# Performance work log

Measured on AMD Instinct MI355X. Metric: run time of the kernel, lower is better.

## Reference

```python
import jax, jax.numpy as jnp
import numpy as np
import math

B, S, D = 4096, 16, 256
HS, HT, O = 512, 512, 1


def setup_inputs() -> dict:
    key = jax.random.key(0)
    ks = jax.random.split(key, 20)
    stdv_s = 1.0 / math.sqrt(HS)
    stdv_t = 1.0 / math.sqrt(HT)
    u = lambda k, shape, s: jax.random.uniform(k, shape, jnp.float32, -s, s)
    return {
        "X": jax.random.normal(ks[0], (B, S, D), jnp.float32),
        # SpatialLSTM params (init uniform(-1/sqrt(H), 1/sqrt(H)) as in torch)
        "sa_W": u(ks[1], (D, 4 * HS), stdv_s),
        "sa_U": u(ks[2], (HS, 4 * HS), stdv_s),
        "sa_b": u(ks[3], (4 * HS,), stdv_s),
        "sa_Wa": u(ks[4], (D, D), stdv_s),
        "sa_Ua": u(ks[5], (2 * HS, D), stdv_s),
        "sa_ba": u(ks[6], (D,), stdv_s),
        "sa_Va": u(ks[7], (D, D), stdv_s),
        # TemporalLSTM params
        "ta_Wa": u(ks[8], (HS, S), stdv_t),
        "ta_Ua": u(ks[9], (HT, S), stdv_t),
        "ta_ba": u(ks[10], (S,), stdv_t),
        "ta_Va": u(ks[11], (S, S), stdv_t),
        "ta_W": u(ks[12], (HS, 4 * HT), stdv_t),
        "ta_U": u(ks[13], (HT, 4 * HT), stdv_t),
        "ta_b": u(ks[14], (4 * HT,), stdv_t),
        "ta_Wy": u(ks[15], (O, 4 * HT), stdv_t),
        "fc_W": u(ks[16], (O, HT), stdv_t),
        "fc_b": u(ks[17], (O,), stdv_t),
    }


def _lstm_update(gates, c, H):
    i = jax.nn.sigmoid(gates[:, :H])
    f = jax.nn.sigmoid(gates[:, H:2 * H])
    g = jnp.tanh(gates[:, 2 * H:3 * H])
    o = jax.nn.sigmoid(gates[:, 3 * H:])
    c_new = f * c + i * g
    h_new = o * jnp.tanh(c_new)
    return h_new, c_new


def _forward(X, sa_W, sa_U, sa_b, sa_Wa, sa_Ua, sa_ba, sa_Va,
             ta_Wa, ta_Ua, ta_ba, ta_Va, ta_W, ta_U, ta_b, ta_Wy, fc_W, fc_b):
    batch = X.shape[0]
    x = X  # x = X[:, :, 0:input_dim] == full X
    y0 = X[:, 0, D - 1:D]  # y = X[:, :, input_dim-1:], take t=0 -> [B, 1]

    # ---- Spatial attention LSTM over time ----
    def sa_step(carry, x_t):
        h, c = carry
        hc = jnp.concatenate([h, c], axis=1)  # [B, 2*HS]
        a_t = jnp.tanh(x_t @ sa_Wa + hc @ sa_Ua + sa_ba) @ sa_Va  # [B, D]
        alpha_t = jax.nn.softmax(a_t, axis=1)
        xt = alpha_t * x_t
        gates = xt @ sa_W + h @ sa_U + sa_b  # [B, 4*HS]
        h, c = _lstm_update(gates, c, HS)
        return (h, c), h

    h0 = jnp.zeros((batch, HS), X.dtype)
    c0 = jnp.zeros((batch, HS), X.dtype)
    _, hseq = jax.lax.scan(sa_step, (h0, c0), jnp.swapaxes(x, 0, 1))  # [S, B, HS]
    H3 = jnp.swapaxes(hseq, 0, 1)  # [B, S, HS]

    # ---- Temporal attention LSTM ----
    s0 = jnp.zeros((batch, HT), X.dtype)  # s_t is never updated in the original code

    def ta_step(carry, h_t):
        lh, lc, y_prev = carry
        beta = jnp.tanh(h_t @ ta_Wa + s0 @ ta_Ua + ta_ba) @ ta_Va  # [B, S]
        beta = jax.nn.softmax(beta, axis=1)
        h_ctx = jnp.einsum('bs,bsh->bh', beta, H3)  # [B, HS]
        gates = h_ctx @ ta_W + lh @ ta_U + y_prev @ ta_Wy + ta_b  # [B, 4*HT]
        lh, lc = _lstm_update(gates, lc, HT)
        y = lh @ fc_W.T + fc_b  # [B, O]
        return (lh, lc, y), None

    (_, _, y_pred), _ = jax.lax.scan(ta_step, (h0[:, :HT] * 0.0, c0[:, :HT] * 0.0, y0), hseq)
    return y_pred  # [B, O]


def reference(X, sa_W, sa_U, sa_b, sa_Wa, sa_Ua, sa_ba, sa_Va,
              ta_Wa, ta_Ua, ta_ba, ta_Va, ta_W, ta_U, ta_b, ta_Wy, fc_W, fc_b):
    return _forward(X, sa_W, sa_U, sa_b, sa_Wa, sa_Ua, sa_ba, sa_Va,
                    ta_Wa, ta_Ua, ta_ba, ta_Va, ta_W, ta_U, ta_b, ta_Wy, fc_W, fc_b)
```

## Files before the change

kernel.cpp:

```cpp
#include <hip/hip_runtime.h>


constexpr int Bb = 4096;
constexpr int Ss = 16;
constexpr int Dd = 256;
constexpr int Hh = 512;

typedef __attribute__((ext_vector_type(8))) short short8;
typedef __attribute__((ext_vector_type(4))) float f32x4;

__device__ __forceinline__ float sigm(float x) { return 1.0f / (1.0f + expf(-x)); }

__device__ __forceinline__ unsigned short f2bf(float x) {
    unsigned int u = __float_as_uint(x);
    u = (u + 0x7fffu + ((u >> 16) & 1u)) >> 16;
    return (unsigned short)u;
}
__device__ __forceinline__ float bf2f(unsigned short h) {
    return __uint_as_float(((unsigned int)h) << 16);
}
__device__ __forceinline__ void async16(const void* g, void* l) {
    __builtin_amdgcn_global_load_lds(
        (const __attribute__((address_space(1))) void*)g,
        (__attribute__((address_space(3))) void*)l, 16, 0, 0);
}

struct SegB { const unsigned short* Ah; const unsigned short* Al;
              const unsigned short* Bh; const unsigned short* Bl;
              int lda; int ldb; int K; };

template<int BM, int BN, int NSEG, int EPI>
__global__ __launch_bounds__(256) void gemm_mfma_k(
    SegB s0, SegB s1, SegB s2,
    const float* __restrict__ bias,
    float* __restrict__ C,
    unsigned short* __restrict__ Th, unsigned short* __restrict__ Tl,
    int ldc)
{
    constexpr int WM = BM / 2, WN = BN / 2;
    constexpr int FI = WM / 16, FJ = WN / 16;
    __shared__ __align__(16) unsigned short sA[2][BM * 32];
    __shared__ __align__(16) unsigned short sB[2][BN * 32];
    const int tid  = threadIdx.x;
    const int lane = tid & 63;
    const int wv   = tid >> 6;
    const int wm   = wv & 1, wn = wv >> 1;
    const int row0 = blockIdx.x * BM;
    const int col0 = blockIdx.y * BN;

    f32x4 acc[FI][FJ];
#pragma unroll
    for (int i = 0; i < FI; i++)
#pragma unroll
        for (int j = 0; j < FJ; j++) acc[i][j] = (f32x4){0.f, 0.f, 0.f, 0.f};

    const int lrow = lane >> 2;
    const int lcol = (lane & 3) * 8;
    const int q8   = (lane >> 4) * 8;
    const int l15  = lane & 15;

#pragma unroll
    for (int sgi = 0; sgi < NSEG; ++sgi) {
        const SegB sg = (sgi == 0) ? s0 : ((sgi == 1) ? s1 : s2);
        const int K = sg.K;
        for (int k0 = 0; k0 < K; k0 += 32) {
#pragma unroll
            for (int c = wv; c < BM / 16; c += 4) {
                const int r = c * 16 + lrow;
                const size_t gA = (size_t)(row0 + r) * sg.lda + k0 + lcol;
                const int lo = c * 512 + lane * 8;
                async16(sg.Ah + gA, &sA[0][lo]);
                async16(sg.Al + gA, &sA[1][lo]);
            }
#pragma unroll
            for (int c = wv; c < BN / 16; c += 4) {
                const int r = c * 16 + lrow;
                const size_t gB = (size_t)(col0 + r) * sg.ldb + k0 + lcol;
                const int lo = c * 512 + lane * 8;
                async16(sg.Bh + gB, &sB[0][lo]);
                async16(sg.Bl + gB, &sB[1][lo]);
            }
            __syncthreads();
            short8 ah[FI], al[FI], bh[FJ], bl[FJ];
#pragma unroll
            for (int i = 0; i < FI; i++) {
                const int m = wm * WM + i * 16 + l15;
                ah[i] = *reinterpret_cast<const short8*>(&sA[0][m * 32 + q8]);
                al[i] = *reinterpret_cast<const short8*>(&sA[1][m * 32 + q8]);
            }
#pragma unroll
            for (int j = 0; j < FJ; j++) {
                const int n = wn * WN + j * 16 + l15;
                bh[j] = *reinterpret_cast<const short8*>(&sB[0][n * 32 + q8]);
                bl[j] = *reinterpret_cast<const short8*>(&sB[1][n * 32 + q8]);
            }
#pragma unroll
            for (int i = 0; i < FI; i++)
#pragma unroll
                for (int j = 0; j < FJ; j++) {
                    acc[i][j] = __builtin_amdgcn_mfma_f32_16x16x32_bf16(ah[i], bh[j], acc[i][j], 0, 0, 0);
                    acc[i][j] = __builtin_amdgcn_mfma_f32_16x16x32_bf16(ah[i], bl[j], acc[i][j], 0, 0, 0);
                    acc[i][j] = __builtin_amdgcn_mfma_f32_16x16x32_bf16(al[i], bh[j], acc[i][j], 0, 0, 0);
                }
            __syncthreads();
        }
    }
#pragma unroll
    for (int i = 0; i < FI; i++) {
#pragma unroll
        for (int j = 0; j < FJ; j++) {
            const int col = col0 + wn * WN + j * 16 + l15;
#pragma unroll
            for (int r = 0; r < 4; r++) {
                const int row = row0 + wm * WM + i * 16 + (lane >> 4) * 4 + r;
                float v = acc[i][j][r];
                if (EPI == 1) {
                    v = tanhf(v + bias[col]);
                    unsigned short hb = f2bf(v);
                    Th[(size_t)row * ldc + col] = hb;
                    Tl[(size_t)row * ldc + col] = f2bf(v - bf2f(hb));
                } else {
                    C[(size_t)row * ldc + col] = v;
                }
            }
        }
    }
}

__global__ __launch_bounds__(256) void splitT_k(const float* __restrict__ W,
                                                unsigned short* __restrict__ Th,
                                                unsigned short* __restrict__ Tl,
                                                int Kd, int Nd)
{
    __shared__ float tile[32][33];
    const int bk = blockIdx.x * 32, bn = blockIdx.y * 32;
    const int tid = threadIdx.x;
    const int r = tid >> 3, c4 = (tid & 7) * 4;
    const float4 v = *reinterpret_cast<const float4*>(&W[(size_t)(bk + r) * Nd + bn + c4]);
    tile[r][c4 + 0] = v.x; tile[r][c4 + 1] = v.y;
    tile[r][c4 + 2] = v.z; tile[r][c4 + 3] = v.w;
    __syncthreads();
    const int n = r, k4 = c4;
    ushort4 hq, lq;
    unsigned short* hp = (unsigned short*)&hq;
    unsigned short* lp = (unsigned short*)&lq;
#pragma unroll
    for (int q = 0; q < 4; q++) {
        float x = tile[k4 + q][n];
        unsigned short h = f2bf(x);
        hp[q] = h;
        lp[q] = f2bf(x - bf2f(h));
    }
    *reinterpret_cast<ushort4*>(&Th[(size_t)(bn + n) * Kd + bk + k4]) = hq;
    *reinterpret_cast<ushort4*>(&Tl[(size_t)(bn + n) * Kd + bk + k4]) = lq;
}

__global__ __launch_bounds__(256) void init_k(const float* __restrict__ X,
                                              unsigned short* __restrict__ xsh,
                                              unsigned short* __restrict__ xsl,
                                              float* __restrict__ yv)
{
    int idx = blockIdx.x * 256 + threadIdx.x;
    int b = idx >> 8, d = idx & 255;
    float xv = X[(size_t)b * (Ss * Dd) + d];
    unsigned short hb = f2bf(xv);
    xsh[idx] = hb;
    xsl[idx] = f2bf(xv - bf2f(hb));
    if (d == Dd - 1) yv[b] = xv;
}

__global__ __launch_bounds__(256) void softmax_xt_k(const float* __restrict__ a,
                                                    const float* __restrict__ X,
                                                    unsigned short* __restrict__ xh,
                                                    unsigned short* __restrict__ xl,
                                                    int t)
{
    int b = blockIdx.x, tid = threadIdx.x;
    __shared__ float red[256];
    float v = a[(size_t)b * Dd + tid];
    red[tid] = v; __syncthreads();
    for (int s = 128; s > 0; s >>= 1) {
        if (tid < s) red[tid] = fmaxf(red[tid], red[tid + s]);
        __syncthreads();
    }
    float mx = red[0]; __syncthreads();
    float e = expf(v - mx);
    red[tid] = e; __syncthreads();
    for (int s = 128; s > 0; s >>= 1) {
        if (tid < s) red[tid] += red[tid + s];
        __syncthreads();
    }
    float inv = 1.0f / red[0];
    float xv = e * inv * X[(size_t)b * Ss * Dd + (size_t)t * Dd + tid];
    unsigned short h = f2bf(xv);
    xh[(size_t)b * Dd + tid] = h;
    xl[(size_t)b * Dd + tid] = f2bf(xv - bf2f(h));
}

template<int ZC, int SPLITX>
__global__ __launch_bounds__(256) void lstm_sa_k(
    const float* __restrict__ gates, const float* __restrict__ bias,
    float* __restrict__ c_io,
    unsigned short* __restrict__ h3h, unsigned short* __restrict__ h3l,
    unsigned short* __restrict__ ch, unsigned short* __restrict__ cl,
    const float* __restrict__ X,
    unsigned short* __restrict__ xsh, unsigned short* __restrict__ xsl,
    int tnext)
{
    int idx = blockIdx.x * 256 + threadIdx.x;
    int b = idx >> 9, j = idx & 511;
    const float* g = gates + (size_t)b * 4 * Hh;
    float gi = g[j]          + bias[j];
    float gf = g[Hh + j]     + bias[Hh + j];
    float gg = g[2 * Hh + j] + bias[2 * Hh + j];
    float go = g[3 * Hh + j] + bias[3 * Hh + j];
    float i_ = sigm(gi), f_ = sigm(gf), gv = tanhf(gg), o_ = sigm(go);
    float cp = ZC ? 0.0f : c_io[idx];
    float c = f_ * cp + i_ * gv;
    c_io[idx] = c;
    unsigned short cb = f2bf(c);
    ch[idx] = cb;
    cl[idx] = f2bf(c - bf2f(cb));
    float h = o_ * tanhf(c);
    unsigned short hb = f2bf(h);
    h3h[idx] = hb;
    h3l[idx] = f2bf(h - bf2f(hb));
    if (SPLITX && j < Dd) {
        float xv = X[(size_t)b * (Ss * Dd) + (size_t)tnext * Dd + j];
        unsigned short xb = f2bf(xv);
        xsh[(size_t)b * Dd + j] = xb;
        xsl[(size_t)b * Dd + j] = f2bf(xv - bf2f(xb));
    }
}

template<int ZC>
__global__ __launch_bounds__(512) void lstm_ta_k(const float* __restrict__ gates,
                                                 const float* __restrict__ bias,
                                                 const float* __restrict__ wy,
                                                 const float* __restrict__ fcW,
                                                 const float* __restrict__ fcb,
                                                 float* __restrict__ yv,
                                                 float* __restrict__ c_io,
                                                 unsigned short* __restrict__ hh,
                                                 unsigned short* __restrict__ hl,
                                                 float* __restrict__ outp)
{
    int b = blockIdx.x, j = threadIdx.x;
    size_t idx = (size_t)b * Hh + j;
    const float* g = gates + (size_t)b * 4 * Hh;
    float yb = yv[b];
    float gi = g[j]          + bias[j]          + yb * wy[j];
    float gf = g[Hh + j]     + bias[Hh + j]     + yb * wy[Hh + j];
    float gg = g[2 * Hh + j] + bias[2 * Hh + j] + yb * wy[2 * Hh + j];
    float go = g[3 * Hh + j] + bias[3 * Hh + j] + yb * wy[3 * Hh + j];
    float i_ = sigm(gi), f_ = sigm(gf), gv = tanhf(gg), o_ = sigm(go);
    float cp = ZC ? 0.0f : c_io[idx];
    float c = f_ * cp + i_ * gv;
    c_io[idx] = c;
    float h = o_ * tanhf(c);
    unsigned short hb = f2bf(h);
    hh[idx] = hb;
    hl[idx] = f2bf(h - bf2f(hb));
    float p = h * fcW[j];
#pragma unroll
    for (int off = 32; off > 0; off >>= 1) p += __shfl_down(p, off, 64);
    __shared__ float wred[8];
    if ((j & 63) == 0) wred[j >> 6] = p;
    __syncthreads();
    if (j == 0) {
        float y = fcb[0];
#pragma unroll
        for (int w = 0; w < 8; w++) y += wred[w];
        yv[b] = y;
        if (outp) outp[b] = y;
    }
}

__global__ __launch_bounds__(256) void beta_k(const unsigned short* __restrict__ H3h,
                                              const unsigned short* __restrict__ H3l,
                                              const float* __restrict__ taWa,
                                              const float* __restrict__ taba,
                                              const float* __restrict__ taVa,
                                              float* __restrict__ beta)
{
    int bx = blockIdx.x, t = blockIdx.y, tid = threadIdx.x;
    __shared__ float Was[512 * 16];
    __shared__ float red[16 * 16 * 16];
    __shared__ float Vas[256];
    __shared__ float tt[16][17];
    __shared__ float lt[16][17];
    for (int i = tid; i < 512 * 16; i += 256) Was[i] = taWa[i];
    Vas[tid] = taVa[tid];
    __syncthreads();
    const int r = tid >> 4, c = tid & 15;
    const int b = bx * 16 + r;
    const unsigned short* hrh = H3h + ((size_t)t * Bb + b) * Hh + c * 32;
    const unsigned short* hrl = H3l + ((size_t)t * Bb + b) * Hh + c * 32;
    float acc[16];
#pragma unroll
    for (int n = 0; n < 16; n++) acc[n] = 0.0f;
    for (int k = 0; k < 32; k++) {
        float hk = bf2f(hrh[k]) + bf2f(hrl[k]);
        const float* w = &Was[(c * 32 + k) * 16];
#pragma unroll
        for (int n = 0; n < 16; n++) acc[n] = fmaf(hk, w[n], acc[n]);
    }
#pragma unroll
    for (int n = 0; n < 16; n++) red[(r * 16 + n) * 16 + c] = acc[n];
    __syncthreads();
    float s = 0.0f;
#pragma unroll
    for (int cc = 0; cc < 16; cc++) s += red[(r * 16 + c) * 16 + cc];
    tt[r][c] = tanhf(s + taba[c]);
    __syncthreads();
    float l = 0.0f;
#pragma unroll
    for (int m = 0; m < 16; m++) l = fmaf(tt[r][m], Vas[m * 16 + c], l);
    lt[r][c] = l;
    __syncthreads();
    float mx = -1e30f;
#pragma unroll
    for (int m = 0; m < 16; m++) mx = fmaxf(mx, lt[r][m]);
    float sum = 0.0f;
#pragma unroll
    for (int m = 0; m < 16; m++) sum += expf(lt[r][m] - mx);
    beta[((size_t)t * Bb + b) * 16 + c] = expf(l - mx) / sum;
}

__global__ __launch_bounds__(256) void hctx_all_k(unsigned short* __restrict__ H3h,
                                                  unsigned short* __restrict__ H3l,
                                                  const float* __restrict__ beta)
{
    int b = blockIdx.x, tid = threadIdx.x;
    __shared__ float Hs[16][516];
    __shared__ float bs[16][16];
    for (int i = tid; i < 16 * 512; i += 256) {
        int s = i >> 9, h = i & 511;
        size_t o = ((size_t)s * Bb + b) * Hh + h;
        Hs[s][h] = bf2f(H3h[o]) + bf2f(H3l[o]);
    }
    {
        int t = tid >> 4, s = tid & 15;
        bs[t][s] = beta[((size_t)t * Bb + b) * 16 + s];
    }
    __syncthreads();
#pragma unroll
    for (int t = 0; t < 16; t++) {
        for (int h = tid; h < Hh; h += 256) {
            float a = 0.0f;
#pragma unroll
            for (int s = 0; s < 16; s++) a = fmaf(bs[t][s], Hs[s][h], a);
            unsigned short hb = f2bf(a);
            size_t o = ((size_t)t * Bb + b) * Hh + h;
            H3h[o] = hb;
            H3l[o] = f2bf(a - bf2f(hb));
        }
    }
}

extern "C" void kernel_launch(void* const* d_in, const int* in_sizes, int n_in,
                              void* d_out, int out_size, void* d_ws, size_t ws_size,
                              hipStream_t stream)
{
    (void)in_sizes; (void)n_in; (void)out_size; (void)ws_size;
    const float* X     = (const float*)d_in[0];
    const float* sa_W  = (const float*)d_in[1];
    const float* sa_U  = (const float*)d_in[2];
    const float* sa_b  = (const float*)d_in[3];
    const float* sa_Wa = (const float*)d_in[4];
    const float* sa_Ua = (const float*)d_in[5];
    const float* sa_ba = (const float*)d_in[6];
    const float* sa_Va = (const float*)d_in[7];
    const float* ta_Wa = (const float*)d_in[8];
    const float* ta_ba = (const float*)d_in[10];
    const float* ta_Va = (const float*)d_in[11];
    const float* ta_W  = (const float*)d_in[12];
    const float* ta_U  = (const float*)d_in[13];
    const float* ta_b  = (const float*)d_in[14];
    const float* ta_Wy = (const float*)d_in[15];
    const float* fc_W  = (const float*)d_in[16];
    const float* fc_b  = (const float*)d_in[17];

    char* base = (char*)d_ws;
    size_t off = 0;
    auto alloc = [&](size_t bytes) {
        void* p = base + off; off += (bytes + 255) & ~(size_t)255; return p;
    };
    const size_t BH = (size_t)Bb * Hh;
    float* gates = (float*)alloc(BH * 4 * 4);
    float* avxt  = gates;
    unsigned short* H3h = (unsigned short*)alloc((size_t)Ss * BH * 2);
    unsigned short* H3l = (unsigned short*)alloc((size_t)Ss * BH * 2);
    float* cbuf = (float*)alloc(BH * 4);
    float* lc   = (float*)alloc(BH * 4);
    unsigned short* xth = (unsigned short*)alloc((size_t)Bb * Dd * 2);
    unsigned short* xtl = (unsigned short*)alloc((size_t)Bb * Dd * 2);
    unsigned short* xsh = (unsigned short*)alloc((size_t)Bb * Dd * 2);
    unsigned short* xsl = (unsigned short*)alloc((size_t)Bb * Dd * 2);
    unsigned short* ch  = (unsigned short*)alloc(BH * 2);
    unsigned short* cl  = (unsigned short*)alloc(BH * 2);
    unsigned short* tmph = (unsigned short*)alloc((size_t)Bb * Dd * 2);
    unsigned short* tmpl = (unsigned short*)alloc((size_t)Bb * Dd * 2);
    unsigned short* saWth = (unsigned short*)alloc((size_t)Dd * 4 * Hh * 2);
    unsigned short* saWtl = (unsigned short*)alloc((size_t)Dd * 4 * Hh * 2);
    unsigned short* saUth = (unsigned short*)alloc((size_t)Hh * 4 * Hh * 2);
    unsigned short* saUtl = (unsigned short*)alloc((size_t)Hh * 4 * Hh * 2);
    unsigned short* taWth = (unsigned short*)alloc((size_t)Hh * 4 * Hh * 2);
    unsigned short* taWtl = (unsigned short*)alloc((size_t)Hh * 4 * Hh * 2);
    unsigned short* taUth = (unsigned short*)alloc((size_t)Hh * 4 * Hh * 2);
    unsigned short* taUtl = (unsigned short*)alloc((size_t)Hh * 4 * Hh * 2);
    unsigned short* WaTh = (unsigned short*)alloc((size_t)Dd * Dd * 2);
    unsigned short* WaTl = (unsigned short*)alloc((size_t)Dd * Dd * 2);
    unsigned short* UaTh = (unsigned short*)alloc((size_t)2 * Hh * Dd * 2);
    unsigned short* UaTl = (unsigned short*)alloc((size_t)2 * Hh * Dd * 2);
    unsigned short* VaTh = (unsigned short*)alloc((size_t)Dd * Dd * 2);
    unsigned short* VaTl = (unsigned short*)alloc((size_t)Dd * Dd * 2);
    float* yv = (float*)alloc((size_t)Bb * 4);
    float* beta = (float*)xth;
    unsigned short* lhh = (unsigned short*)cbuf;
    unsigned short* lhl = (unsigned short*)cbuf + BH;

    splitT_k<<<dim3(Dd / 32, (4 * Hh) / 32), 256, 0, stream>>>(sa_W, saWth, saWtl, Dd, 4 * Hh);
    splitT_k<<<dim3(Hh / 32, (4 * Hh) / 32), 256, 0, stream>>>(sa_U, saUth, saUtl, Hh, 4 * Hh);
    splitT_k<<<dim3(Hh / 32, (4 * Hh) / 32), 256, 0, stream>>>(ta_W, taWth, taWtl, Hh, 4 * Hh);
    splitT_k<<<dim3(Hh / 32, (4 * Hh) / 32), 256, 0, stream>>>(ta_U, taUth, taUtl, Hh, 4 * Hh);
    splitT_k<<<dim3(Dd / 32, Dd / 32), 256, 0, stream>>>(sa_Wa, WaTh, WaTl, Dd, Dd);
    splitT_k<<<dim3((2 * Hh) / 32, Dd / 32), 256, 0, stream>>>(sa_Ua, UaTh, UaTl, 2 * Hh, Dd);
    splitT_k<<<dim3(Dd / 32, Dd / 32), 256, 0, stream>>>(sa_Va, VaTh, VaTl, Dd, Dd);
    init_k<<<dim3((Bb * Dd) / 256), 256, 0, stream>>>(X, xsh, xsl, yv);

    const dim3 agrid(Bb / 64, Dd / 64);
    const dim3 ggrid(Bb / 128, (4 * Hh) / 128);

    for (int t = 0; t < Ss; ++t) {
        SegB a0{ xsh, xsl, WaTh, WaTl, Dd, Dd, Dd };
        if (t == 0) {
            gemm_mfma_k<64, 64, 1, 1><<<agrid, 256, 0, stream>>>(
                a0, a0, a0, sa_ba, nullptr, tmph, tmpl, Dd);
        } else {
            SegB a1{ H3h + (size_t)(t - 1) * BH, H3l + (size_t)(t - 1) * BH,
                     UaTh, UaTl, Hh, 2 * Hh, Hh };
            SegB a2{ ch, cl, UaTh + Hh, UaTl + Hh, Hh, 2 * Hh, Hh };
            gemm_mfma_k<64, 64, 3, 1><<<agrid, 256, 0, stream>>>(
                a0, a1, a2, sa_ba, nullptr, tmph, tmpl, Dd);
        }

        SegB v0{ tmph, tmpl, VaTh, VaTl, Dd, Dd, Dd };
        gemm_mfma_k<64, 64, 1, 0><<<agrid, 256, 0, stream>>>(
            v0, v0, v0, nullptr, avxt, nullptr, nullptr, Dd);

        softmax_xt_k<<<Bb, 256, 0, stream>>>(avxt, X, xth, xtl, t);

        SegB g0{ xth, xtl, saWth, saWtl, Dd, Dd, Dd };
        if (t == 0) {
            gemm_mfma_k<128, 128, 1, 0><<<ggrid, 256, 0, stream>>>(
                g0, g0, g0, nullptr, gates, nullptr, nullptr, 4 * Hh);
            lstm_sa_k<1, 1><<<(int)(BH / 256), 256, 0, stream>>>(
                gates, sa_b, cbuf, H3h + (size_t)t * BH, H3l + (size_t)t * BH,
                ch, cl, X, xsh, xsl, t + 1);
        } else {
            SegB g1{ H3h + (size_t)(t - 1) * BH, H3l + (size_t)(t - 1) * BH,
                     saUth, saUtl, Hh, Hh, Hh };
            gemm_mfma_k<128, 128, 2, 0><<<ggrid, 256, 0, stream>>>(
                g0, g1, g1, nullptr, gates, nullptr, nullptr, 4 * Hh);
            if (t < Ss - 1)
                lstm_sa_k<0, 1><<<(int)(BH / 256), 256, 0, stream>>>(
                    gates, sa_b, cbuf, H3h + (size_t)t * BH, H3l + (size_t)t * BH,
                    ch, cl, X, xsh, xsl, t + 1);
            else
                lstm_sa_k<0, 0><<<(int)(BH / 256), 256, 0, stream>>>(
                    gates, sa_b, cbuf, H3h + (size_t)t * BH, H3l + (size_t)t * BH,
                    ch, cl, X, xsh, xsl, 0);
        }
    }

    beta_k<<<dim3(Bb / 16, Ss), 256, 0, stream>>>(H3h, H3l, ta_Wa, ta_ba, ta_Va, beta);
    hctx_all_k<<<Bb, 256, 0, stream>>>(H3h, H3l, beta);

    for (int t = 0; t < Ss; ++t) {
        SegB g0{ H3h + (size_t)t * BH, H3l + (size_t)t * BH,
                 taWth, taWtl, Hh, Hh, Hh };
        if (t == 0) {
            gemm_mfma_k<128, 128, 1, 0><<<ggrid, 256, 0, stream>>>(
                g0, g0, g0, nullptr, gates, nullptr, nullptr, 4 * Hh);
            lstm_ta_k<1><<<Bb, 512, 0, stream>>>(
                gates, ta_b, ta_Wy, fc_W, fc_b, yv, lc, lhh, lhl,
                (t == Ss - 1) ? (float*)d_out : nullptr);
        } else {
            SegB g1{ lhh, lhl, taUth, taUtl, Hh, Hh, Hh };
            gemm_mfma_k<128, 128, 2, 0><<<ggrid, 256, 0, stream>>>(
                g0, g1, g1, nullptr, gates, nullptr, nullptr, 4 * Hh);
            lstm_ta_k<0><<<Bb, 512, 0, stream>>>(
                gates, ta_b, ta_Wy, fc_W, fc_b, yv, lc, lhh, lhl,
                (t == Ss - 1) ? (float*)d_out : nullptr);
        }
    }
}
```

Baseline: 2.916 ms.

## Fuse LSTM gate GEMMs with cell update epilogue and MFMA-ize temporal attention

Adds a gate GEMM kernel whose tile interleaves the four gate columns for each hidden unit, so the LSTM cell update runs in the epilogue. This removes the fp32 gates buffer round trip and the separate lstm kernels for both recurrences. The temporal attention beta computation now uses split-bf16 MFMA over 128-row tiles with a pre-transposed Wa, and the x split-copy moves into the softmax kernel. The temporal hidden state is double-buffered because the fused kernel reads the previous h while writing the new one, and a small y_k kernel computes the fc output. The cost is a larger per-thread epilogue and a narrow 32-column tile.

```diff
diff --git a/kernel.cpp b/kernel.cpp
--- a/kernel.cpp
+++ b/kernel.cpp
@@ -122,6 +122,121 @@
                 } else {
                     C[(size_t)row * ldc + col] = v;
                 }
+            }
+        }
+    }
+}
+
+template<int NSEG, int ZC, int TA>
+__global__ __launch_bounds__(256) void gemm_gates_k(
+    SegB s0, SegB s1,
+    const float* __restrict__ bias,
+    const float* __restrict__ wy,
+    const float* __restrict__ yv,
+    float* __restrict__ c_io,
+    unsigned short* __restrict__ hh, unsigned short* __restrict__ hl,
+    unsigned short* __restrict__ ch, unsigned short* __restrict__ cl)
+{
+    __shared__ __align__(16) unsigned short sA[2][128 * 32];
+    __shared__ __align__(16) unsigned short sB[2][128 * 32];
+    const int tid  = threadIdx.x;
+    const int lane = tid & 63;
+    const int wv   = tid >> 6;
+    const int wm   = wv & 1, wn = wv >> 1;
+    const int row0 = blockIdx.x * 128;
+    const int by32 = blockIdx.y * 32;
+
+    f32x4 acc[4][4];
+#pragma unroll
+    for (int i = 0; i < 4; i++)
+#pragma unroll
+        for (int g = 0; g < 4; g++) acc[i][g] = (f32x4){0.f, 0.f, 0.f, 0.f};
+
+    const int lrow = lane >> 2;
+    const int lcol = (lane & 3) * 8;
+    const int q8   = (lane >> 4) * 8;
+    const int l15  = lane & 15;
+
+#pragma unroll
+    for (int sgi = 0; sgi < NSEG; ++sgi) {
+        const SegB sg = (sgi == 0) ? s0 : s1;
+        const int K = sg.K;
+        for (int k0 = 0; k0 < K; k0 += 32) {
+#pragma unroll
+            for (int c = wv; c < 8; c += 4) {
+                const int r = c * 16 + lrow;
+                const size_t gA = (size_t)(row0 + r) * sg.lda + k0 + lcol;
+                const int lo = c * 512 + lane * 8;
+                async16(sg.Ah + gA, &sA[0][lo]);
+                async16(sg.Al + gA, &sA[1][lo]);
+            }
+#pragma unroll
+            for (int cc = wv; cc < 8; cc += 4) {
+                const int g  = cc >> 1;
+                const int jj = (cc & 1) * 16 + lrow;
+                const int rowg = g * 512 + by32 + jj;
+                const size_t gB = (size_t)rowg * sg.ldb + k0 + lcol;
+                const int lo = cc * 512 + lane * 8;
+                async16(sg.Bh + gB, &sB[0][lo]);
+                async16(sg.Bl + gB, &sB[1][lo]);
+            }
+            __syncthreads();
+            short8 ah[4], al[4], bh[4], bl[4];
+#pragma unroll
+            for (int i = 0; i < 4; i++) {
+                const int m = wm * 64 + i * 16 + l15;
+                ah[i] = *reinterpret_cast<const short8*>(&sA[0][m * 32 + q8]);
+                al[i] = *reinterpret_cast<const short8*>(&sA[1][m * 32 + q8]);
+            }
+#pragma unroll
+            for (int g = 0; g < 4; g++) {
+                const int n = g * 32 + wn * 16 + l15;
+                bh[g] = *reinterpret_cast<const short8*>(&sB[0][n * 32 + q8]);
+                bl[g] = *reinterpret_cast<const short8*>(&sB[1][n * 32 + q8]);
+            }
+#pragma unroll
+            for (int i = 0; i < 4; i++)
+#pragma unroll
+                for (int g = 0; g < 4; g++) {
+                    acc[i][g] = __builtin_amdgcn_mfma_f32_16x16x32_bf16(ah[i], bh[g], acc[i][g], 0, 0, 0);
+                    acc[i][g] = __builtin_amdgcn_mfma_f32_16x16x32_bf16(ah[i], bl[g], acc[i][g], 0, 0, 0);
+                    acc[i][g] = __builtin_amdgcn_mfma_f32_16x16x32_bf16(al[i], bh[g], acc[i][g], 0, 0, 0);
+                }
+            __syncthreads();
+        }
+    }
+    const int j = by32 + wn * 16 + l15;
+    const float b0 = bias[j],            b1 = bias[Hh + j];
+    const float b2 = bias[2 * Hh + j],   b3 = bias[3 * Hh + j];
+    float w0 = 0.f, w1 = 0.f, w2 = 0.f, w3 = 0.f;
+    if (TA) { w0 = wy[j]; w1 = wy[Hh + j]; w2 = wy[2 * Hh + j]; w3 = wy[3 * Hh + j]; }
+#pragma unroll
+    for (int i = 0; i < 4; i++) {
+        const int rbase = row0 + wm * 64 + i * 16 + (lane >> 4) * 4;
+#pragma unroll
+        for (int r = 0; r < 4; r++) {
+            const int row = rbase + r;
+            float gi = acc[i][0][r] + b0;
+            float gf = acc[i][1][r] + b1;
+            float gg = acc[i][2][r] + b2;
+            float go = acc[i][3][r] + b3;
+            if (TA) {
+                const float yb = yv[row];
+                gi += yb * w0; gf += yb * w1; gg += yb * w2; go += yb * w3;
+            }
+            const float i_ = sigm(gi), f_ = sigm(gf), gv = tanhf(gg), o_ = sigm(go);
+            const size_t idx = (size_t)row * Hh + j;
+            const float cp = ZC ? 0.0f : c_io[idx];
+            const float c = f_ * cp + i_ * gv;
+            c_io[idx] = c;
+            const float h = o_ * tanhf(c);
+            const unsigned short hb = f2bf(h);
+            hh[idx] = hb;
+            hl[idx] = f2bf(h - bf2f(hb));
+            if (!TA) {
+                const unsigned short cb = f2bf(c);
+                ch[idx] = cb;
+                cl[idx] = f2bf(c - bf2f(cb));
             }
         }
     }
@@ -155,6 +270,18 @@
     *reinterpret_cast<ushort4*>(&Tl[(size_t)(bn + n) * Kd + bk + k4]) = lq;
 }
 
+__global__ __launch_bounds__(256) void splitWa_k(const float* __restrict__ W,
+                                                 unsigned short* __restrict__ Th,
+                                                 unsigned short* __restrict__ Tl)
+{
+    int idx = blockIdx.x * 256 + threadIdx.x;
+    int n = idx >> 9, k = idx & 511;
+    float x = W[(size_t)k * 16 + n];
+    unsigned short h = f2bf(x);
+    Th[idx] = h;
+    Tl[idx] = f2bf(x - bf2f(h));
+}
+
 __global__ __launch_bounds__(256) void init_k(const float* __restrict__ X,
                                               unsigned short* __restrict__ xsh,
                                               unsigned short* __restrict__ xsl,
@@ -169,10 +296,13 @@
     if (d == Dd - 1) yv[b] = xv;
 }
 
+template<int SPLITX>
 __global__ __launch_bounds__(256) void softmax_xt_k(const float* __restrict__ a,
                                                     const float* __restrict__ X,
                                                     unsigned short* __restrict__ xh,
                                                     unsigned short* __restrict__ xl,
+                                                    unsigned short* __restrict__ xsh,
+                                                    unsigned short* __restrict__ xsl,
                                                     int t)
 {
     int b = blockIdx.x, tid = threadIdx.x;
@@ -195,136 +325,107 @@
     unsigned short h = f2bf(xv);
     xh[(size_t)b * Dd + tid] = h;
     xl[(size_t)b * Dd + tid] = f2bf(xv - bf2f(h));
-}
-
-template<int ZC, int SPLITX>
-__global__ __launch_bounds__(256) void lstm_sa_k(
-    const float* __restrict__ gates, const float* __restrict__ bias,
-    float* __restrict__ c_io,
-    unsigned short* __restrict__ h3h, unsigned short* __restrict__ h3l,
-    unsigned short* __restrict__ ch, unsigned short* __restrict__ cl,
-    const float* __restrict__ X,
-    unsigned short* __restrict__ xsh, unsigned short* __restrict__ xsl,
-    int tnext)
-{
-    int idx = blockIdx.x * 256 + threadIdx.x;
-    int b = idx >> 9, j = idx & 511;
-    const float* g = gates + (size_t)b * 4 * Hh;
-    float gi = g[j]          + bias[j];
-    float gf = g[Hh + j]     + bias[Hh + j];
-    float gg = g[2 * Hh + j] + bias[2 * Hh + j];
-    float go = g[3 * Hh + j] + bias[3 * Hh + j];
-    float i_ = sigm(gi), f_ = sigm(gf), gv = tanhf(gg), o_ = sigm(go);
-    float cp = ZC ? 0.0f : c_io[idx];
-    float c = f_ * cp + i_ * gv;
-    c_io[idx] = c;
-    unsigned short cb = f2bf(c);
-    ch[idx] = cb;
-    cl[idx] = f2bf(c - bf2f(cb));
-    float h = o_ * tanhf(c);
-    unsigned short hb = f2bf(h);
-    h3h[idx] = hb;
-    h3l[idx] = f2bf(h - bf2f(hb));
-    if (SPLITX && j < Dd) {
-        float xv = X[(size_t)b * (Ss * Dd) + (size_t)tnext * Dd + j];
-        unsigned short xb = f2bf(xv);
-        xsh[(size_t)b * Dd + j] = xb;
-        xsl[(size_t)b * Dd + j] = f2bf(xv - bf2f(xb));
-    }
-}
-
-template<int ZC>
-__global__ __launch_bounds__(512) void lstm_ta_k(const float* __restrict__ gates,
-                                                 const float* __restrict__ bias,
-                                                 const float* __restrict__ wy,
-                                                 const float* __restrict__ fcW,
-                                                 const float* __restrict__ fcb,
-                                                 float* __restrict__ yv,
-                                                 float* __restrict__ c_io,
-                                                 unsigned short* __restrict__ hh,
-                                                 unsigned short* __restrict__ hl,
-                                                 float* __restrict__ outp)
-{
-    int b = blockIdx.x, j = threadIdx.x;
-    size_t idx = (size_t)b * Hh + j;
-    const float* g = gates + (size_t)b * 4 * Hh;
-    float yb = yv[b];
-    float gi = g[j]          + bias[j]          + yb * wy[j];
-    float gf = g[Hh + j]     + bias[Hh + j]     + yb * wy[Hh + j];
-    float gg = g[2 * Hh + j] + bias[2 * Hh + j] + yb * wy[2 * Hh + j];
-    float go = g[3 * Hh + j] + bias[3 * Hh + j] + yb * wy[3 * Hh + j];
-    float i_ = sigm(gi), f_ = sigm(gf), gv = tanhf(gg), o_ = sigm(go);
-    float cp = ZC ? 0.0f : c_io[idx];
-    float c = f_ * cp + i_ * gv;
-    c_io[idx] = c;
-    float h = o_ * tanhf(c);
-    unsigned short hb = f2bf(h);
-    hh[idx] = hb;
-    hl[idx] = f2bf(h - bf2f(hb));
-    float p = h * fcW[j];
-#pragma unroll
-    for (int off = 32; off > 0; off >>= 1) p += __shfl_down(p, off, 64);
-    __shared__ float wred[8];
-    if ((j & 63) == 0) wred[j >> 6] = p;
-    __syncthreads();
-    if (j == 0) {
-        float y = fcb[0];
-#pragma unroll
-        for (int w = 0; w < 8; w++) y += wred[w];
-        yv[b] = y;
-        if (outp) outp[b] = y;
+    if (SPLITX) {
+        float xn = X[(size_t)b * Ss * Dd + (size_t)(t + 1) * Dd + tid];
+        unsigned short xb = f2bf(xn);
+        xsh[(size_t)b * Dd + tid] = xb;
+        xsl[(size_t)b * Dd + tid] = f2bf(xn - bf2f(xb));
     }
 }
 
 __global__ __launch_bounds__(256) void beta_k(const unsigned short* __restrict__ H3h,
                                               const unsigned short* __restrict__ H3l,
-                                              const float* __restrict__ taWa,
+                                              const unsigned short* __restrict__ WaTh,
+                                              const unsigned short* __restrict__ WaTl,
                                               const float* __restrict__ taba,
                                               const float* __restrict__ taVa,
                                               float* __restrict__ beta)
 {
-    int bx = blockIdx.x, t = blockIdx.y, tid = threadIdx.x;
-    __shared__ float Was[512 * 16];
-    __shared__ float red[16 * 16 * 16];
+    __shared__ __align__(16) unsigned short sW[2][16 * 512];
+    __shared__ __align__(16) unsigned short sA[2][128 * 32];
+    __shared__ float tt[128][17];
     __shared__ float Vas[256];
-    __shared__ float tt[16][17];
-    __shared__ float lt[16][17];
-    for (int i = tid; i < 512 * 16; i += 256) Was[i] = taWa[i];
+    const int tid  = threadIdx.x;
+    const int lane = tid & 63;
+    const int wv   = tid >> 6;
+    const int lrow = lane >> 2;
+    const int lcol = (lane & 3) * 8;
+    const int q8   = (lane >> 4) * 8;
+    const int l15  = lane & 15;
+    const size_t row0 = (size_t)blockIdx.x * 128;
+
+#pragma unroll
+    for (int it = 0; it < 4; ++it) {
+        const int lo = wv * 2048 + it * 512 + lane * 8;
+        async16(WaTh + lo, &sW[0][lo]);
+        async16(WaTl + lo, &sW[1][lo]);
+    }
     Vas[tid] = taVa[tid];
+
+    f32x4 acc[2];
+    acc[0] = (f32x4){0.f, 0.f, 0.f, 0.f};
+    acc[1] = (f32x4){0.f, 0.f, 0.f, 0.f};
+
+    for (int kc = 0; kc < 16; ++kc) {
+        const int k0 = kc * 32;
+#pragma unroll
+        for (int c = wv; c < 8; c += 4) {
+            const int r = c * 16 + lrow;
+            const size_t gA = (row0 + r) * Hh + k0 + lcol;
+            const int lo = c * 512 + lane * 8;
+            async16(H3h + gA, &sA[0][lo]);
+            async16(H3l + gA, &sA[1][lo]);
+        }
+        __syncthreads();
+        const short8 bh = *reinterpret_cast<const short8*>(&sW[0][l15 * 512 + k0 + q8]);
+        const short8 bl = *reinterpret_cast<const short8*>(&sW[1][l15 * 512 + k0 + q8]);
+#pragma unroll
+        for (int i = 0; i < 2; i++) {
+            const int m = wv * 32 + i * 16 + l15;
+            const short8 ah = *reinterpret_cast<const short8*>(&sA[0][m * 32 + q8]);
+            const short8 al = *reinterpret_cast<const short8*>(&sA[1][m * 32 + q8]);
+            acc[i] = __builtin_amdgcn_mfma_f32_16x16x32_bf16(ah, bh, acc[i], 0, 0, 0);
+            acc[i] = __builtin_amdgcn_mfma_f32_16x16x32_bf16(ah, bl, acc[i], 0, 0, 0);
+            acc[i] = __builtin_amdgcn_mfma_f32_16x16x32_bf16(al, bh, acc[i], 0, 0, 0);
+        }
+        __syncthreads();
+    }
+    const float ba = taba[l15];
+#pragma unroll
+    for (int i = 0; i < 2; i++) {
+#pragma unroll
+        for (int r = 0; r < 4; r++) {
+            const int rl = wv * 32 + i * 16 + (lane >> 4) * 4 + r;
+            tt[rl][l15] = tanhf(acc[i][r] + ba);
+        }
+    }
     __syncthreads();
-    const int r = tid >> 4, c = tid & 15;
-    const int b = bx * 16 + r;
-    const unsigned short* hrh = H3h + ((size_t)t * Bb + b) * Hh + c * 32;
-    const unsigned short* hrl = H3l + ((size_t)t * Bb + b) * Hh + c * 32;
-    float acc[16];
-#pragma unroll
-    for (int n = 0; n < 16; n++) acc[n] = 0.0f;
-    for (int k = 0; k < 32; k++) {
-        float hk = bf2f(hrh[k]) + bf2f(hrl[k]);
-        const float* w = &Was[(c * 32 + k) * 16];
-#pragma unroll
-        for (int n = 0; n < 16; n++) acc[n] = fmaf(hk, w[n], acc[n]);
-    }
-#pragma unroll
-    for (int n = 0; n < 16; n++) red[(r * 16 + n) * 16 + c] = acc[n];
-    __syncthreads();
-    float s = 0.0f;
-#pragma unroll
-    for (int cc = 0; cc < 16; cc++) s += red[(r * 16 + c) * 16 + cc];
-    tt[r][c] = tanhf(s + taba[c]);
-    __syncthreads();
-    float l = 0.0f;
-#pragma unroll
-    for (int m = 0; m < 16; m++) l = fmaf(tt[r][m], Vas[m * 16 + c], l);
-    lt[r][c] = l;
-    __syncthreads();
-    float mx = -1e30f;
-#pragma unroll
-    for (int m = 0; m < 16; m++) mx = fmaxf(mx, lt[r][m]);
-    float sum = 0.0f;
-#pragma unroll
-    for (int m = 0; m < 16; m++) sum += expf(lt[r][m] - mx);
-    beta[((size_t)t * Bb + b) * 16 + c] = expf(l - mx) / sum;
+    if (tid < 128) {
+        float tv[16];
+#pragma unroll
+        for (int m = 0; m < 16; m++) tv[m] = tt[tid][m];
+        float l[16];
+        float mx = -1e30f;
+#pragma unroll
+        for (int n = 0; n < 16; n++) {
+            float s = 0.0f;
+#pragma unroll
+            for (int m = 0; m < 16; m++) s = fmaf(tv[m], Vas[m * 16 + n], s);
+            l[n] = s;
+            mx = fmaxf(mx, s);
+        }
+        float sum = 0.0f;
+#pragma unroll
+        for (int n = 0; n < 16; n++) { l[n] = expf(l[n] - mx); sum += l[n]; }
+        const float inv = 1.0f / sum;
+        float* bp = beta + (row0 + tid) * 16;
+#pragma unroll
+        for (int n4 = 0; n4 < 4; n4++) {
+            float4 v = { l[n4 * 4] * inv, l[n4 * 4 + 1] * inv,
+                         l[n4 * 4 + 2] * inv, l[n4 * 4 + 3] * inv };
+            *reinterpret_cast<float4*>(bp + n4 * 4) = v;
+        }
+    }
 }
 
 __global__ __launch_bounds__(256) void hctx_all_k(unsigned short* __restrict__ H3h,
@@ -355,6 +456,30 @@
             H3h[o] = hb;
             H3l[o] = f2bf(a - bf2f(hb));
         }
+    }
+}
+
+__global__ __launch_bounds__(256) void y_k(const unsigned short* __restrict__ hh,
+                                           const unsigned short* __restrict__ hl,
+                                           const float* __restrict__ fcW,
+                                           const float* __restrict__ fcb,
+                                           float* __restrict__ yv,
+                                           float* __restrict__ outp)
+{
+    int b = blockIdx.x, tid = threadIdx.x;
+    size_t o = (size_t)b * Hh + tid;
+    float h0 = bf2f(hh[o]) + bf2f(hl[o]);
+    float h1 = bf2f(hh[o + 256]) + bf2f(hl[o + 256]);
+    float p = h0 * fcW[tid] + h1 * fcW[tid + 256];
+#pragma unroll
+    for (int off = 32; off > 0; off >>= 1) p += __shfl_down(p, off, 64);
+    __shared__ float wred[4];
+    if ((tid & 63) == 0) wred[tid >> 6] = p;
+    __syncthreads();
+    if (tid == 0) {
+        float y = fcb[0] + wred[0] + wred[1] + wred[2] + wred[3];
+        yv[b] = y;
+        if (outp) outp[b] = y;
     }
 }
 
@@ -387,12 +512,13 @@
         void* p = base + off; off += (bytes + 255) & ~(size_t)255; return p;
     };
     const size_t BH = (size_t)Bb * Hh;
-    float* gates = (float*)alloc(BH * 4 * 4);
-    float* avxt  = gates;
+    float* avxt = (float*)alloc((size_t)Bb * Dd * 4);
     unsigned short* H3h = (unsigned short*)alloc((size_t)Ss * BH * 2);
     unsigned short* H3l = (unsigned short*)alloc((size_t)Ss * BH * 2);
     float* cbuf = (float*)alloc(BH * 4);
     float* lc   = (float*)alloc(BH * 4);
+    unsigned short* lhBh = (unsigned short*)alloc(BH * 2);
+    unsigned short* lhBl = (unsigned short*)alloc(BH * 2);
     unsigned short* xth = (unsigned short*)alloc((size_t)Bb * Dd * 2);
     unsigned short* xtl = (unsigned short*)alloc((size_t)Bb * Dd * 2);
     unsigned short* xsh = (unsigned short*)alloc((size_t)Bb * Dd * 2);
@@ -415,10 +541,14 @@
     unsigned short* UaTl = (unsigned short*)alloc((size_t)2 * Hh * Dd * 2);
     unsigned short* VaTh = (unsigned short*)alloc((size_t)Dd * Dd * 2);
     unsigned short* VaTl = (unsigned short*)alloc((size_t)Dd * Dd * 2);
+    unsigned short* tWaTh = (unsigned short*)alloc((size_t)16 * Hh * 2);
+    unsigned short* tWaTl = (unsigned short*)alloc((size_t)16 * Hh * 2);
     float* yv = (float*)alloc((size_t)Bb * 4);
     float* beta = (float*)xth;
-    unsigned short* lhh = (unsigned short*)cbuf;
-    unsigned short* lhl = (unsigned short*)cbuf + BH;
+    unsigned short* lhAh = (unsigned short*)cbuf;
+    unsigned short* lhAl = (unsigned short*)cbuf + BH;
+    unsigned short* lhh[2] = { lhAh, lhBh };
+    unsigned short* lhl[2] = { lhAl, lhBl };
 
     splitT_k<<<dim3(Dd / 32, (4 * Hh) / 32), 256, 0, stream>>>(sa_W, saWth, saWtl, Dd, 4 * Hh);
     splitT_k<<<dim3(Hh / 32, (4 * Hh) / 32), 256, 0, stream>>>(sa_U, saUth, saUtl, Hh, 4 * Hh);
@@ -427,10 +557,11 @@
     splitT_k<<<dim3(Dd / 32, Dd / 32), 256, 0, stream>>>(sa_Wa, WaTh, WaTl, Dd, Dd);
     splitT_k<<<dim3((2 * Hh) / 32, Dd / 32), 256, 0, stream>>>(sa_Ua, UaTh, UaTl, 2 * Hh, Dd);
     splitT_k<<<dim3(Dd / 32, Dd / 32), 256, 0, stream>>>(sa_Va, VaTh, VaTl, Dd, Dd);
+    splitWa_k<<<dim3(32), 256, 0, stream>>>(ta_Wa, tWaTh, tWaTl);
     init_k<<<dim3((Bb * Dd) / 256), 256, 0, stream>>>(X, xsh, xsl, yv);
 
     const dim3 agrid(Bb / 64, Dd / 64);
-    const dim3 ggrid(Bb / 128, (4 * Hh) / 128);
+    const dim3 ggrid(Bb / 128, Hh / 32);
 
     for (int t = 0; t < Ss; ++t) {
         SegB a0{ xsh, xsl, WaTh, WaTl, Dd, Dd, Dd };
@@ -449,50 +580,42 @@
         gemm_mfma_k<64, 64, 1, 0><<<agrid, 256, 0, stream>>>(
             v0, v0, v0, nullptr, avxt, nullptr, nullptr, Dd);
 
-        softmax_xt_k<<<Bb, 256, 0, stream>>>(avxt, X, xth, xtl, t);
+        if (t < Ss - 1)
+            softmax_xt_k<1><<<Bb, 256, 0, stream>>>(avxt, X, xth, xtl, xsh, xsl, t);
+        else
+            softmax_xt_k<0><<<Bb, 256, 0, stream>>>(avxt, X, xth, xtl, xsh, xsl, t);
 
         SegB g0{ xth, xtl, saWth, saWtl, Dd, Dd, Dd };
         if (t == 0) {
-            gemm_mfma_k<128, 128, 1, 0><<<ggrid, 256, 0, stream>>>(
-                g0, g0, g0, nullptr, gates, nullptr, nullptr, 4 * Hh);
-            lstm_sa_k<1, 1><<<(int)(BH / 256), 256, 0, stream>>>(
-                gates, sa_b, cbuf, H3h + (size_t)t * BH, H3l + (size_t)t * BH,
-                ch, cl, X, xsh, xsl, t + 1);
+            gemm_gates_k<1, 1, 0><<<ggrid, 256, 0, stream>>>(
+                g0, g0, sa_b, nullptr, nullptr, cbuf,
+                H3h + (size_t)t * BH, H3l + (size_t)t * BH, ch, cl);
         } else {
             SegB g1{ H3h + (size_t)(t - 1) * BH, H3l + (size_t)(t - 1) * BH,
                      saUth, saUtl, Hh, Hh, Hh };
-            gemm_mfma_k<128, 128, 2, 0><<<ggrid, 256, 0, stream>>>(
-                g0, g1, g1, nullptr, gates, nullptr, nullptr, 4 * Hh);
-            if (t < Ss - 1)
-                lstm_sa_k<0, 1><<<(int)(BH / 256), 256, 0, stream>>>(
-                    gates, sa_b, cbuf, H3h + (size_t)t * BH, H3l + (size_t)t * BH,
-                    ch, cl, X, xsh, xsl, t + 1);
-            else
-                lstm_sa_k<0, 0><<<(int)(BH / 256), 256, 0, stream>>>(
-                    gates, sa_b, cbuf, H3h + (size_t)t * BH, H3l + (size_t)t * BH,
-                    ch, cl, X, xsh, xsl, 0);
-        }
-    }
-
-    beta_k<<<dim3(Bb / 16, Ss), 256, 0, stream>>>(H3h, H3l, ta_Wa, ta_ba, ta_Va, beta);
+            gemm_gates_k<2, 0, 0><<<ggrid, 256, 0, stream>>>(
+                g0, g1, sa_b, nullptr, nullptr, cbuf,
+                H3h + (size_t)t * BH, H3l + (size_t)t * BH, ch, cl);
+        }
+    }
+
+    beta_k<<<dim3((Ss * Bb) / 128), 256, 0, stream>>>(
+        H3h, H3l, tWaTh, tWaTl, ta_ba, ta_Va, beta);
     hctx_all_k<<<Bb, 256, 0, stream>>>(H3h, H3l, beta);
 
     for (int t = 0; t < Ss; ++t) {
         SegB g0{ H3h + (size_t)t * BH, H3l + (size_t)t * BH,
                  taWth, taWtl, Hh, Hh, Hh };
+        const int po = t & 1;
         if (t == 0) {
-            gemm_mfma_k<128, 128, 1, 0><<<ggrid, 256, 0, stream>>>(
-                g0, g0, g0, nullptr, gates, nullptr, nullptr, 4 * Hh);
-            lstm_ta_k<1><<<Bb, 512, 0, stream>>>(
-                gates, ta_b, ta_Wy, fc_W, fc_b, yv, lc, lhh, lhl,
-                (t == Ss - 1) ? (float*)d_out : nullptr);
+            gemm_gates_k<1, 1, 1><<<ggrid, 256, 0, stream>>>(
+                g0, g0, ta_b, ta_Wy, yv, lc, lhh[0], lhl[0], nullptr, nullptr);
         } else {
-            SegB g1{ lhh, lhl, taUth, taUtl, Hh, Hh, Hh };
-            gemm_mfma_k<128, 128, 2, 0><<<ggrid, 256, 0, stream>>>(
-                g0, g1, g1, nullptr, gates, nullptr, nullptr, 4 * Hh);
-            lstm_ta_k<0><<<Bb, 512, 0, stream>>>(
-                gates, ta_b, ta_Wy, fc_W, fc_b, yv, lc, lhh, lhl,
-                (t == Ss - 1) ? (float*)d_out : nullptr);
-        }
-    }
-}
+            SegB g1{ lhh[(t - 1) & 1], lhl[(t - 1) & 1], taUth, taUtl, Hh, Hh, Hh };
+            gemm_gates_k<2, 0, 1><<<ggrid, 256, 0, stream>>>(
+                g0, g1, ta_b, ta_Wy, yv, lc, lhh[po], lhl[po], nullptr, nullptr);
+        }
+        y_k<<<Bb, 256, 0, stream>>>(lhh[po], lhl[po], fc_W, fc_b, yv,
+                                    (t == Ss - 1) ? (float*)d_out : nullptr);
+    }
+}
```

Result: faster. 2.493 ms (-14.5%).
